# Kernel optimization log

Measured on AMD Instinct MI355X. Metric: run time of the kernel, lower is better.

The kernel has to match this reference:

```python
import jax, jax.numpy as jnp
import numpy as np

MATRIC_TYPE = 0   # 0: corr, 1: cov
WEIGHT_IN = 1.0
WEIGHT_BET = 1.0


def setup_inputs() -> dict:
    key = jax.random.key(0)
    k1, k2, k3 = jax.random.split(key, 3)
    x = jax.random.normal(k1, (256, 128, 768), dtype=jnp.float32)
    label = jax.random.randint(k2, (256,), 0, 1000, dtype=jnp.int64 if jax.config.read('jax_enable_x64') else jnp.int32)
    genre_label = jax.random.randint(k3, (256,), 0, 8, dtype=jnp.int64 if jax.config.read('jax_enable_x64') else jnp.int32)
    return {"x": x, "label": label, "genre_label": genre_label}


def _compute_various(x):
    # x: [B, N, D] -> within (D,D), between (D,D)
    B, N, D = x.shape
    tol_num = B * N
    x_mean = jnp.mean(x, axis=1)                       # (B, D)
    mean = jnp.mean(x.reshape(-1, D), axis=0)          # (D,)
    res_x = x - x_mean[:, None, :]                     # (B, N, D)
    # fused batched scatter accumulation (replaces python loop of small mms)
    within = jnp.einsum('bnd,bne->de', res_x, res_x) / tol_num
    res_mean = x_mean - mean                           # (B, D)
    between = (N * (res_mean.T @ res_mean)) / tol_num
    return within, between


def _corr_normalize(m):
    # torch code: Diag=(d,1); mm(Diag.T, Diag)=(1,1) scalar = sum(diag^2)
    d = jnp.diagonal(m)
    s = jnp.sqrt(jnp.sum(d * d))
    return m / s


def reference(x, label, genre_label):
    input_x = x[::2]
    input_u = x[1::2]
    x1_within, x1_between = _compute_various(input_x)
    x2_within, x2_between = _compute_various(input_u)
    if MATRIC_TYPE == 0:
        x1_within = _corr_normalize(x1_within)
        x2_within = _corr_normalize(x2_within)
        x1_between = _corr_normalize(x1_between)
        x2_between = _corr_normalize(x2_between)
    within = jnp.sum((x1_within - x2_within) ** 2)
    between = jnp.sum((x1_between - x2_between) ** 2)
    return WEIGHT_IN * within + WEIGHT_BET * between
```

## Files before the change

kernel.cpp:

```cpp
#include <hip/hip_runtime.h>


typedef float f32x2 __attribute__((ext_vector_type(2)));
typedef float f32x4 __attribute__((ext_vector_type(4)));
typedef short bf16x8 __attribute__((ext_vector_type(8)));
typedef unsigned short u16x4 __attribute__((ext_vector_type(4)));

static constexpr size_t OFF_RT    = 0;
static constexpr size_t OFF_XM    = 50331648;
static constexpr size_t OFF_M     = 51118080;
static constexpr size_t OFF_RM    = 51124224;
static constexpr size_t OFF_P2    = 51517440;
static constexpr size_t OFF_BPART = 54269952;
static constexpr size_t OFF_P1    = 54355968;

__device__ __forceinline__ unsigned int f2bf_u32(float f) {
  union { float f; unsigned int u; } v; v.f = f;
  unsigned int u = v.u;
  unsigned int lsb = (u >> 16) & 1u;
  u += 0x7fffu + lsb;
  return u >> 16;
}

__device__ __forceinline__ void gload_lds16(const void* g, void* l) {
  __builtin_amdgcn_global_load_lds(
      (const __attribute__((address_space(1))) unsigned int*)g,
      (__attribute__((address_space(3))) unsigned int*)l, 16, 0, 0);
}

__global__ void __launch_bounds__(256) k1_means_convert(const float* __restrict__ x,
                                                        float* __restrict__ xm,
                                                        unsigned short* __restrict__ RT) {
  __shared__ unsigned short T[128][130];
  __shared__ float pm[4][128];
  int bid = blockIdx.x;
  int dt = bid % 6, borig = bid / 6;
  int s = borig & 1, b = borig >> 1;
  int tid = threadIdx.x, w = tid >> 6, lane = tid & 63;

  const float* xb = x + (size_t)borig * (128 * 768) + dt * 128 + 2 * lane;
  float cs0 = 0.f, cs1 = 0.f;
#pragma unroll
  for (int g = 0; g < 8; ++g) {
    int n0 = w * 32 + g * 4;
    f32x2 a0 = *reinterpret_cast<const f32x2*>(xb + (size_t)(n0 + 0) * 768);
    f32x2 a1 = *reinterpret_cast<const f32x2*>(xb + (size_t)(n0 + 1) * 768);
    f32x2 a2 = *reinterpret_cast<const f32x2*>(xb + (size_t)(n0 + 2) * 768);
    f32x2 a3 = *reinterpret_cast<const f32x2*>(xb + (size_t)(n0 + 3) * 768);
    cs0 += a0[0] + a1[0] + a2[0] + a3[0];
    cs1 += a0[1] + a1[1] + a2[1] + a3[1];
    u16x4 p0, p1;
    p0[0] = (unsigned short)f2bf_u32(a0[0]); p0[1] = (unsigned short)f2bf_u32(a1[0]);
    p0[2] = (unsigned short)f2bf_u32(a2[0]); p0[3] = (unsigned short)f2bf_u32(a3[0]);
    p1[0] = (unsigned short)f2bf_u32(a0[1]); p1[1] = (unsigned short)f2bf_u32(a1[1]);
    p1[2] = (unsigned short)f2bf_u32(a2[1]); p1[3] = (unsigned short)f2bf_u32(a3[1]);
    *reinterpret_cast<u16x4*>(&T[2 * lane + 0][n0]) = p0;
    *reinterpret_cast<u16x4*>(&T[2 * lane + 1][n0]) = p1;
  }
  *reinterpret_cast<f32x2*>(&pm[w][2 * lane]) = f32x2{cs0, cs1};
  __syncthreads();

  if (tid < 128) {
    float mv = (pm[0][tid] + pm[1][tid] + pm[2][tid] + pm[3][tid]) * (1.f / 128.f);
    xm[((size_t)(s * 128 + b)) * 768ull + dt * 128 + tid] = mv;
  }

  int half = lane >> 5;
  int nb = (lane & 31) * 4;
  unsigned short* rtbase = RT + (size_t)s * (768ull * 16384ull) + (size_t)(b * 128 + nb);
#pragma unroll
  for (int i = 0; i < 16; ++i) {
    int d_loc = w * 32 + 2 * i + half;
    uint2 v = *reinterpret_cast<const uint2*>(&T[d_loc][nb]);
    *reinterpret_cast<uint2*>(rtbase + (size_t)(dt * 128 + d_loc) * 16384ull) = v;
  }
}

__global__ void __launch_bounds__(256) k2_slice_mean(const float* __restrict__ xm,
                                                     float* __restrict__ m,
                                                     unsigned short* __restrict__ rmT) {
  __shared__ float pm[4][64];
  __shared__ float ml[64];
  int s = blockIdx.x / 12, dg = blockIdx.x % 12;
  int t = threadIdx.x;
  int d_loc = t & 63, part = t >> 6;
  int d = dg * 64 + d_loc;
  const float* base = xm + (size_t)s * 128ull * 768ull + d;
  float acc = 0.f;
#pragma unroll 4
  for (int i = 0; i < 32; ++i) acc += base[(size_t)(part * 32 + i) * 768ull];
  pm[part][d_loc] = acc;
  __syncthreads();
  if (t < 64) {
    float mv = (pm[0][t] + pm[1][t] + pm[2][t] + pm[3][t]) * (1.f / 128.f);
    m[s * 768 + dg * 64 + t] = mv;
    ml[t] = mv;
  }
  __syncthreads();
  float mv = ml[d_loc];
  unsigned short* rt = rmT + ((size_t)s * 768ull + d) * 128ull + part * 32;
#pragma unroll 4
  for (int i = 0; i < 32; ++i)
    rt[i] = (unsigned short)f2bf_u32(base[(size_t)(part * 32 + i) * 768ull] - mv);
}

__device__ __forceinline__ void stage_tile(const unsigned short* __restrict__ g, int KP, int k0,
                                           unsigned short* lds, int wave, int lane) {
#pragma unroll
  for (int i = 0; i < 4; ++i) {
    int cb = (i * 4 + wave) * 64;
    int chunk = cb + lane;
    int r = chunk >> 3, sl = chunk & 7;
    int ss = sl ^ (r & 7);
    const unsigned short* src = g + (size_t)r * KP + (k0 + ss * 8);
    gload_lds16(src, lds + (size_t)cb * 8);
  }
}

__device__ __forceinline__ bf16x8 read_frag(const unsigned short* lds, int row, int slot) {
  int chunk = row * 8 + (slot ^ (row & 7));
  return *reinterpret_cast<const bf16x8*>(lds + chunk * 8);
}

__device__ __forceinline__ void tp2tile(int tp, int& td, int& te) {
  td = 0; int t2 = tp;
  while (t2 >= 6 - td) { t2 -= 6 - td; ++td; }
  te = td + t2;
}

__global__ void __launch_bounds__(256) gemm_ata(const unsigned short* __restrict__ Rbig,
                                                const unsigned short* __restrict__ rmT,
                                                float* __restrict__ P1, float* __restrict__ P2,
                                                int ksplit) {
  __shared__ unsigned short Ta[2][128 * 64];
  __shared__ unsigned short Tb[2][128 * 64];
  int bid = blockIdx.x;
  int nbig = 42 * ksplit;
  const unsigned short* R; size_t slice_stride; int KP;
  int s, tp, step0, step1; float* pout;
  if (bid < nbig) {
    int logical;
    if (nbig == 504) logical = (bid & 7) * 63 + (bid >> 3);
    else             logical = bid;
    int g = logical / 21; tp = logical % 21;
    s = g & 1; int c = g >> 1;
    R = Rbig; slice_stride = 768ull * 16384ull; KP = 16384;
    step0 = (256 * c) / ksplit; step1 = (256 * (c + 1)) / ksplit;
    pout = P1 + (size_t)((tp * 2 + s) * ksplit + c) * (128 * 128);
  } else {
    int b2 = bid - nbig;
    R = rmT; slice_stride = 768ull * 128ull; KP = 128;
    s = b2 & 1; tp = b2 >> 1; step0 = 0; step1 = 2;
    pout = P2 + (size_t)b2 * (128 * 128);
  }
  int td, te; tp2tile(tp, td, te);
  bool diag = (td == te);
  const unsigned short* Ra = R + (size_t)s * slice_stride + (size_t)(td * 128) * KP;
  const unsigned short* Rb = R + (size_t)s * slice_stride + (size_t)(te * 128) * KP;
  int tid = threadIdx.x, wave = tid >> 6, lane = tid & 63;
  int m_off = (wave >> 1) * 64, n_off = (wave & 1) * 64;
  int row_a = m_off + (lane & 15), row_b = n_off + (lane & 15);
  f32x4 acc[4][4];
#pragma unroll
  for (int i = 0; i < 4; ++i)
#pragma unroll
    for (int j = 0; j < 4; ++j) { acc[i][j][0]=0.f; acc[i][j][1]=0.f; acc[i][j][2]=0.f; acc[i][j][3]=0.f; }

  stage_tile(Ra, KP, step0 * 64, Ta[0], wave, lane);
  if (!diag) stage_tile(Rb, KP, step0 * 64, Tb[0], wave, lane);
  __syncthreads();

  int cur = 0;
  for (int kt = step0; kt < step1; ++kt) {
    if (kt + 1 < step1) {
      stage_tile(Ra, KP, (kt + 1) * 64, Ta[cur ^ 1], wave, lane);
      if (!diag) stage_tile(Rb, KP, (kt + 1) * 64, Tb[cur ^ 1], wave, lane);
    }
    const unsigned short* Bsrc = diag ? Ta[cur] : Tb[cur];
#pragma unroll
    for (int ks = 0; ks < 2; ++ks) {
      bf16x8 a[4], b[4];
      int slot = ks * 4 + (lane >> 4);
#pragma unroll
      for (int mi = 0; mi < 4; ++mi) a[mi] = read_frag(Ta[cur], row_a + mi * 16, slot);
#pragma unroll
      for (int ni = 0; ni < 4; ++ni) b[ni] = read_frag(Bsrc, row_b + ni * 16, slot);
#pragma unroll
      for (int mi = 0; mi < 4; ++mi)
#pragma unroll
        for (int ni = 0; ni < 4; ++ni)
          acc[mi][ni] = __builtin_amdgcn_mfma_f32_16x16x32_bf16(a[mi], b[ni], acc[mi][ni], 0, 0, 0);
    }
    __syncthreads();
    cur ^= 1;
  }
  int hi = lane >> 4, lo = lane & 15;
#pragma unroll
  for (int mi = 0; mi < 4; ++mi)
#pragma unroll
    for (int ni = 0; ni < 4; ++ni)
#pragma unroll
      for (int r = 0; r < 4; ++r) {
        int rr = m_off + mi * 16 + hi * 4 + r;
        int cc = n_off + ni * 16 + lo;
        pout[rr * 128 + cc] = acc[mi][ni][r];
      }
}

template <int KS>
__global__ void __launch_bounds__(256) k5_elem(const float* __restrict__ P1,
                                               const float* __restrict__ P2,
                                               const float* __restrict__ m,
                                               float* __restrict__ bpart, int ksplit_rt) {
  __shared__ float red[4][10];
  int bid = blockIdx.x;
  int tp = bid >> 5, sub = bid & 31;
  int td, te; tp2tile(tp, td, te);
  bool diagTile = (td == te);
  float mult = diagTile ? 1.0f : 2.0f;
  int t = threadIdx.x;
  int lane = t & 63, w = t >> 6;
  int ksplit = (KS > 0) ? KS : ksplit_rt;
  float v[10];
#pragma unroll
  for (int j = 0; j < 10; ++j) v[j] = 0.f;

#pragma unroll
  for (int k = 0; k < 2; ++k) {
    int idx = sub * 512 + k * 256 + t;
    int r = idx >> 7, cc = idx & 127;
    int d = td * 128 + r, e = te * 128 + cc;
    float W[2], B[2];
#pragma unroll
    for (int s = 0; s < 2; ++s) {
      const float* base1 = P1 + (size_t)((tp * 2 + s) * ksplit) * 16384ull + idx;
      float g1 = 0.f;
#pragma unroll
      for (int c6 = 0; c6 < ((KS > 0) ? KS : 16); ++c6) {
        if (KS > 0 || c6 < ksplit) g1 += base1[(size_t)c6 * 16384ull];
      }
      float p2v = P2[(size_t)(tp * 2 + s) * 16384ull + idx];
      W[s] = g1 - 128.0f * p2v - 16384.0f * m[s * 768 + d] * m[s * 768 + e];
      B[s] = p2v;
    }
    v[0] += W[0] * W[0] * mult;  v[1] += W[1] * W[1] * mult;  v[2] += W[0] * W[1] * mult;
    v[3] += B[0] * B[0] * mult;  v[4] += B[1] * B[1] * mult;  v[5] += B[0] * B[1] * mult;
    if (diagTile && r == cc) {
      v[6] += W[0] * W[0];  v[7] += W[1] * W[1];
      v[8] += B[0] * B[0];  v[9] += B[1] * B[1];
    }
  }
#pragma unroll
  for (int off = 32; off; off >>= 1)
#pragma unroll
    for (int j = 0; j < 10; ++j) v[j] += __shfl_down(v[j], off, 64);
  if (lane == 0)
#pragma unroll
    for (int j = 0; j < 10; ++j) red[w][j] = v[j];
  __syncthreads();
  if (t < 10) bpart[bid * 16 + t] = red[0][t] + red[1][t] + red[2][t] + red[3][t];
}

__global__ void __launch_bounds__(256) k6_final(const float* __restrict__ bpart,
                                                float* __restrict__ out) {
  __shared__ float red[4][10];
  float acc[10];
#pragma unroll
  for (int j = 0; j < 10; ++j) acc[j] = 0.f;
  for (int i = threadIdx.x; i < 672; i += 256)
#pragma unroll
    for (int j = 0; j < 10; ++j) acc[j] += bpart[i * 16 + j];
  int lane = threadIdx.x & 63, w = threadIdx.x >> 6;
#pragma unroll
  for (int off = 32; off; off >>= 1)
#pragma unroll
    for (int j = 0; j < 10; ++j) acc[j] += __shfl_down(acc[j], off, 64);
  if (lane == 0)
#pragma unroll
    for (int j = 0; j < 10; ++j) red[w][j] = acc[j];
  __syncthreads();
  if (threadIdx.x == 0) {
    float S[10];
#pragma unroll
    for (int j = 0; j < 10; ++j) S[j] = red[0][j] + red[1][j] + red[2][j] + red[3][j];
    float lw = S[0] / S[6] + S[1] / S[7] - 2.0f * S[2] / sqrtf(S[6] * S[7]);
    float lb = S[3] / S[8] + S[4] / S[9] - 2.0f * S[5] / sqrtf(S[8] * S[9]);
    out[0] = lw + lb;
  }
}

extern "C" void kernel_launch(void* const* d_in, const int* in_sizes, int n_in,
                              void* d_out, int out_size, void* d_ws, size_t ws_size,
                              hipStream_t stream) {
  const float* x = (const float*)d_in[0];
  char* ws = (char*)d_ws;
  unsigned short* RT  = (unsigned short*)(ws + OFF_RT);
  float* xm           = (float*)(ws + OFF_XM);
  float* m            = (float*)(ws + OFF_M);
  unsigned short* rmT = (unsigned short*)(ws + OFF_RM);
  float* P2           = (float*)(ws + OFF_P2);
  float* bpart        = (float*)(ws + OFF_BPART);
  float* P1           = (float*)(ws + OFF_P1);
  float* out          = (float*)d_out;

  size_t availP1 = (ws_size > OFF_P1) ? (ws_size - OFF_P1) : 0;
  int ksplit = (int)(availP1 / (42ull * 128 * 128 * 4));
  if (ksplit > 12) ksplit = 12;
  if (ksplit < 1) ksplit = 1;

  hipLaunchKernelGGL(k1_means_convert, dim3(1536), dim3(256), 0, stream, x, xm, RT);
  hipLaunchKernelGGL(k2_slice_mean, dim3(24), dim3(256), 0, stream, xm, m, rmT);
  hipLaunchKernelGGL(gemm_ata, dim3(42 * ksplit + 42), dim3(256), 0, stream,
                     RT, rmT, P1, P2, ksplit);
  if (ksplit == 12) {
    hipLaunchKernelGGL((k5_elem<12>), dim3(672), dim3(256), 0, stream,
                       P1, P2, m, bpart, ksplit);
  } else if (ksplit == 11) {
    hipLaunchKernelGGL((k5_elem<11>), dim3(672), dim3(256), 0, stream,
                       P1, P2, m, bpart, ksplit);
  } else {
    hipLaunchKernelGGL((k5_elem<0>), dim3(672), dim3(256), 0, stream,
                       P1, P2, m, bpart, ksplit);
  }
  hipLaunchKernelGGL(k6_final, dim3(1), dim3(256), 0, stream, bpart, out);
}
```

Before: 71.05 us.

## Fuse slice-mean kernel into between-class GEMM blocks staging from xm

Removes the separate k2_slice_mean launch. The between-class blocks of gemm_ata now compute the per-slice mean for their two 128-column tiles directly from xm, write m from the diagonal blocks, and build the centered bf16 tiles in LDS instead of reading a precomputed rmT buffer. This saves a kernel launch and an intermediate global round trip. In exchange, the mean computation is repeated across tile blocks and the between-class blocks become slower with strided scalar loads, though they are few.

```diff
diff --git a/kernel.cpp b/kernel.cpp
--- a/kernel.cpp
+++ b/kernel.cpp
@@ -9,7 +9,6 @@
 static constexpr size_t OFF_RT    = 0;
 static constexpr size_t OFF_XM    = 50331648;
 static constexpr size_t OFF_M     = 51118080;
-static constexpr size_t OFF_RM    = 51124224;
 static constexpr size_t OFF_P2    = 51517440;
 static constexpr size_t OFF_BPART = 54269952;
 static constexpr size_t OFF_P1    = 54355968;
@@ -76,34 +75,6 @@
   }
 }
 
-__global__ void __launch_bounds__(256) k2_slice_mean(const float* __restrict__ xm,
-                                                     float* __restrict__ m,
-                                                     unsigned short* __restrict__ rmT) {
-  __shared__ float pm[4][64];
-  __shared__ float ml[64];
-  int s = blockIdx.x / 12, dg = blockIdx.x % 12;
-  int t = threadIdx.x;
-  int d_loc = t & 63, part = t >> 6;
-  int d = dg * 64 + d_loc;
-  const float* base = xm + (size_t)s * 128ull * 768ull + d;
-  float acc = 0.f;
-#pragma unroll 4
-  for (int i = 0; i < 32; ++i) acc += base[(size_t)(part * 32 + i) * 768ull];
-  pm[part][d_loc] = acc;
-  __syncthreads();
-  if (t < 64) {
-    float mv = (pm[0][t] + pm[1][t] + pm[2][t] + pm[3][t]) * (1.f / 128.f);
-    m[s * 768 + dg * 64 + t] = mv;
-    ml[t] = mv;
-  }
-  __syncthreads();
-  float mv = ml[d_loc];
-  unsigned short* rt = rmT + ((size_t)s * 768ull + d) * 128ull + part * 32;
-#pragma unroll 4
-  for (int i = 0; i < 32; ++i)
-    rt[i] = (unsigned short)f2bf_u32(base[(size_t)(part * 32 + i) * 768ull] - mv);
-}
-
 __device__ __forceinline__ void stage_tile(const unsigned short* __restrict__ g, int KP, int k0,
                                            unsigned short* lds, int wave, int lane) {
 #pragma unroll
@@ -117,6 +88,23 @@
   }
 }
 
+__device__ __forceinline__ void stage_rm_tile(unsigned short* lds, const float* __restrict__ xmb,
+                                              const float* mlbase, int half, int tid) {
+  for (int c = tid; c < 1024; c += 256) {
+    int r = c >> 3, sl = c & 7, ss = sl ^ (r & 7);
+    int b0 = half * 64 + ss * 8;
+    float mv = mlbase[r];
+    const float* col = xmb + r;
+    u16x4 lo, hi;
+#pragma unroll
+    for (int j = 0; j < 4; ++j) lo[j] = (unsigned short)f2bf_u32(col[(size_t)(b0 + j) * 768] - mv);
+#pragma unroll
+    for (int j = 0; j < 4; ++j) hi[j] = (unsigned short)f2bf_u32(col[(size_t)(b0 + 4 + j) * 768] - mv);
+    u16x4* dst = reinterpret_cast<u16x4*>(lds + (size_t)c * 8);
+    dst[0] = lo; dst[1] = hi;
+  }
+}
+
 __device__ __forceinline__ bf16x8 read_frag(const unsigned short* lds, int row, int slot) {
   int chunk = row * 8 + (slot ^ (row & 7));
   return *reinterpret_cast<const bf16x8*>(lds + chunk * 8);
@@ -129,34 +117,32 @@
 }
 
 __global__ void __launch_bounds__(256) gemm_ata(const unsigned short* __restrict__ Rbig,
-                                                const unsigned short* __restrict__ rmT,
+                                                const float* __restrict__ xm,
+                                                float* __restrict__ mOut,
                                                 float* __restrict__ P1, float* __restrict__ P2,
                                                 int ksplit) {
   __shared__ unsigned short Ta[2][128 * 64];
   __shared__ unsigned short Tb[2][128 * 64];
+  __shared__ float ml[256];
   int bid = blockIdx.x;
   int nbig = 42 * ksplit;
-  const unsigned short* R; size_t slice_stride; int KP;
+  bool isBetween = (bid >= nbig);
   int s, tp, step0, step1; float* pout;
-  if (bid < nbig) {
+  if (!isBetween) {
     int logical;
     if (nbig == 504) logical = (bid & 7) * 63 + (bid >> 3);
     else             logical = bid;
     int g = logical / 21; tp = logical % 21;
     s = g & 1; int c = g >> 1;
-    R = Rbig; slice_stride = 768ull * 16384ull; KP = 16384;
     step0 = (256 * c) / ksplit; step1 = (256 * (c + 1)) / ksplit;
     pout = P1 + (size_t)((tp * 2 + s) * ksplit + c) * (128 * 128);
   } else {
     int b2 = bid - nbig;
-    R = rmT; slice_stride = 768ull * 128ull; KP = 128;
     s = b2 & 1; tp = b2 >> 1; step0 = 0; step1 = 2;
     pout = P2 + (size_t)b2 * (128 * 128);
   }
   int td, te; tp2tile(tp, td, te);
   bool diag = (td == te);
-  const unsigned short* Ra = R + (size_t)s * slice_stride + (size_t)(td * 128) * KP;
-  const unsigned short* Rb = R + (size_t)s * slice_stride + (size_t)(te * 128) * KP;
   int tid = threadIdx.x, wave = tid >> 6, lane = tid & 63;
   int m_off = (wave >> 1) * 64, n_off = (wave & 1) * 64;
   int row_a = m_off + (lane & 15), row_b = n_off + (lane & 15);
@@ -166,13 +152,42 @@
 #pragma unroll
     for (int j = 0; j < 4; ++j) { acc[i][j][0]=0.f; acc[i][j][1]=0.f; acc[i][j][2]=0.f; acc[i][j][3]=0.f; }
 
-  stage_tile(Ra, KP, step0 * 64, Ta[0], wave, lane);
-  if (!diag) stage_tile(Rb, KP, step0 * 64, Tb[0], wave, lane);
+  const unsigned short* Ra = nullptr; const unsigned short* Rb = nullptr;
+  const int KP = 16384;
+  if (!isBetween) {
+    Ra = Rbig + (size_t)s * (768ull * 16384ull) + (size_t)(td * 128) * KP;
+    Rb = Rbig + (size_t)s * (768ull * 16384ull) + (size_t)(te * 128) * KP;
+    stage_tile(Ra, KP, step0 * 64, Ta[0], wave, lane);
+    if (!diag) stage_tile(Rb, KP, step0 * 64, Tb[0], wave, lane);
+  } else {
+    {
+      int tile = (tid < 128) ? td : te;
+      int dl = tid & 127;
+      const float* base = xm + (size_t)s * (128 * 768) + tile * 128 + dl;
+      float a0 = 0.f, a1 = 0.f, a2 = 0.f, a3 = 0.f;
+      for (int b = 0; b < 128; b += 4) {
+        a0 += base[(size_t)(b + 0) * 768]; a1 += base[(size_t)(b + 1) * 768];
+        a2 += base[(size_t)(b + 2) * 768]; a3 += base[(size_t)(b + 3) * 768];
+      }
+      float mv = ((a0 + a1) + (a2 + a3)) * (1.f / 128.f);
+      ml[tid] = mv;
+      if (diag && tid < 128) mOut[s * 768 + td * 128 + dl] = mv;
+    }
+    __syncthreads();
+    const float* xmb_a = xm + (size_t)s * (128 * 768) + td * 128;
+    stage_rm_tile(Ta[0], xmb_a, &ml[0], 0, tid);
+    stage_rm_tile(Ta[1], xmb_a, &ml[0], 1, tid);
+    if (!diag) {
+      const float* xmb_b = xm + (size_t)s * (128 * 768) + te * 128;
+      stage_rm_tile(Tb[0], xmb_b, &ml[128], 0, tid);
+      stage_rm_tile(Tb[1], xmb_b, &ml[128], 1, tid);
+    }
+  }
   __syncthreads();
 
   int cur = 0;
   for (int kt = step0; kt < step1; ++kt) {
-    if (kt + 1 < step1) {
+    if (!isBetween && kt + 1 < step1) {
       stage_tile(Ra, KP, (kt + 1) * 64, Ta[cur ^ 1], wave, lane);
       if (!diag) stage_tile(Rb, KP, (kt + 1) * 64, Tb[cur ^ 1], wave, lane);
     }
@@ -297,7 +312,6 @@
   unsigned short* RT  = (unsigned short*)(ws + OFF_RT);
   float* xm           = (float*)(ws + OFF_XM);
   float* m            = (float*)(ws + OFF_M);
-  unsigned short* rmT = (unsigned short*)(ws + OFF_RM);
   float* P2           = (float*)(ws + OFF_P2);
   float* bpart        = (float*)(ws + OFF_BPART);
   float* P1           = (float*)(ws + OFF_P1);
@@ -309,9 +323,8 @@
   if (ksplit < 1) ksplit = 1;
 
   hipLaunchKernelGGL(k1_means_convert, dim3(1536), dim3(256), 0, stream, x, xm, RT);
-  hipLaunchKernelGGL(k2_slice_mean, dim3(24), dim3(256), 0, stream, xm, m, rmT);
   hipLaunchKernelGGL(gemm_ata, dim3(42 * ksplit + 42), dim3(256), 0, stream,
-                     RT, rmT, P1, P2, ksplit);
+                     RT, xm, m, P1, P2, ksplit);
   if (ksplit == 12) {
     hipLaunchKernelGGL((k5_elem<12>), dim3(672), dim3(256), 0, stream,
                        P1, P2, m, bpart, ksplit);
```

Result: slower. 82.22 us (+15.7%).
